# Optimization experiments

Hardware: AMD Instinct MI355X
Metric: run time of the kernel (lower is better)

Reference implementation:

```python
import jax, jax.numpy as jnp
import numpy as np

B, C, S, H, W = 1, 256, 64, 32, 128
BLOCKS, HEADS, DH = 2, 8, 32
SCALE = DH ** (-0.5)


def layer_norm(x, w, b, eps=1e-5):
    mu = jnp.mean(x, axis=-1, keepdims=True)
    var = jnp.var(x, axis=-1, keepdims=True)
    return (x - mu) * jax.lax.rsqrt(var + eps) * w + b


def generate_y_for_attn(y, u):
    # y: (B,C,H,W), u: (B,S,S) float -> (B, S^2, 2H, C)
    Bv, Cv, Hv, Wv = y.shape
    Sv = u.shape[1]
    uf = jnp.floor(u).reshape(Bv, Sv * Sv)
    u_left = jnp.clip(uf, 0, Wv - 1).astype(jnp.int32)
    u_right = jnp.clip(uf + 1, 0, Wv - 1).astype(jnp.int32)
    yf = y.reshape(Bv, Cv * Hv, Wv)

    def gather_w(idx):
        idxb = jnp.broadcast_to(idx[:, None, :], (Bv, Cv * Hv, Sv * Sv))
        return jnp.take_along_axis(yf, idxb, axis=2).reshape(Bv, Cv, Hv, Sv * Sv)

    ys = jnp.concatenate([gather_w(u_left), gather_w(u_right)], axis=2)  # (B,C,2H,S2)
    return ys.transpose(0, 3, 2, 1)  # (B, S2, 2H, C)


def cross_attention(x, y, p, i):
    # x: (B,M,C), y: (B,M,N,C)
    q = layer_norm(x, p['ln_q_w'][i], p['ln_q_b'][i]) @ p['Wq'][i]        # (B,M,HD)
    k = layer_norm(y, p['ln_k_w'][i], p['ln_k_b'][i]) @ p['Wk'][i]        # (B,M,N,HD)
    v = layer_norm(y, p['ln_v_w'][i], p['ln_v_b'][i]) @ p['Wv'][i]        # (B,M,N,HD)
    Bv, M, _ = q.shape
    N = k.shape[2]
    q = q.reshape(Bv, M, HEADS, DH)
    k = k.reshape(Bv, M, N, HEADS, DH)
    v = v.reshape(Bv, M, N, HEADS, DH)
    dot = SCALE * jnp.einsum('bmhd,bmnhd->bhmn', q, k)                    # (B,H,M,N)
    attn = jax.nn.softmax(dot, axis=-1)
    a = jnp.einsum('bhmn,bmnhd->bmhd', attn, v).reshape(Bv, M, HEADS * DH)
    z = a @ p['Wproj'][i] + p['bproj'][i]
    z = layer_norm(z, p['ln_pre_w'][i], p['ln_pre_b'][i])
    h = jax.nn.gelu(z @ p['Wm1'][i] + p['bm1'][i], approximate=False)
    z = z + (h @ p['Wm2'][i] + p['bm2'][i])
    return layer_norm(z, p['ln_post_w'][i], p['ln_post_b'][i])


def setup_inputs() -> dict:
    key = jax.random.key(0)
    ks = jax.random.split(key, 16)
    std = 0.02
    inp = {
        'grd2sat': jax.random.normal(ks[0], (B, C, S, S), jnp.float32),
        'grd_x': jax.random.normal(ks[1], (B, C, H, W), jnp.float32),
        'u': jax.random.uniform(ks[2], (B, S, S), jnp.float32) * (W - 1),
        'ln_q_w': jnp.ones((BLOCKS, C)), 'ln_q_b': jnp.zeros((BLOCKS, C)),
        'ln_k_w': jnp.ones((BLOCKS, C)), 'ln_k_b': jnp.zeros((BLOCKS, C)),
        'ln_v_w': jnp.ones((BLOCKS, C)), 'ln_v_b': jnp.zeros((BLOCKS, C)),
        'Wq': std * jax.random.normal(ks[3], (BLOCKS, C, HEADS * DH)),
        'Wk': std * jax.random.normal(ks[4], (BLOCKS, C, HEADS * DH)),
        'Wv': std * jax.random.normal(ks[5], (BLOCKS, C, HEADS * DH)),
        'Wproj': std * jax.random.normal(ks[6], (BLOCKS, HEADS * DH, C)),
        'bproj': jnp.zeros((BLOCKS, C)),
        'ln_pre_w': jnp.ones((BLOCKS, C)), 'ln_pre_b': jnp.zeros((BLOCKS, C)),
        'Wm1': std * jax.random.normal(ks[7], (BLOCKS, C, 2 * C)),
        'bm1': jnp.zeros((BLOCKS, 2 * C)),
        'Wm2': std * jax.random.normal(ks[8], (BLOCKS, 2 * C, C)),
        'bm2': jnp.zeros((BLOCKS, C)),
        'ln_post_w': jnp.ones((BLOCKS, C)), 'ln_post_b': jnp.zeros((BLOCKS, C)),
    }
    return inp


def reference(grd2sat, grd_x, u, ln_q_w, ln_q_b, ln_k_w, ln_k_b, ln_v_w, ln_v_b,
              Wq, Wk, Wv, Wproj, bproj, ln_pre_w, ln_pre_b, Wm1, bm1, Wm2, bm2,
              ln_post_w, ln_post_b):
    p = dict(ln_q_w=ln_q_w, ln_q_b=ln_q_b, ln_k_w=ln_k_w, ln_k_b=ln_k_b,
             ln_v_w=ln_v_w, ln_v_b=ln_v_b, Wq=Wq, Wk=Wk, Wv=Wv, Wproj=Wproj,
             bproj=bproj, ln_pre_w=ln_pre_w, ln_pre_b=ln_pre_b, Wm1=Wm1, bm1=bm1,
             Wm2=Wm2, bm2=bm2, ln_post_w=ln_post_w, ln_post_b=ln_post_b)
    y_attn = generate_y_for_attn(grd_x, u)               # (B, S^2, 2H, C)
    x = grd2sat.reshape(B, C, S * S).transpose(0, 2, 1)  # (B, M, C)
    for i in range(BLOCKS):
        # (Swin self-attention layer omitted; cross-attention stack only.)
        x = cross_attention(x, y_attn, p, i)
    out = x.transpose(0, 2, 1).reshape(B, C, S, S)
    # L2 normalize over channel dim
    norm = jnp.sqrt(jnp.sum(out * out, axis=1, keepdims=True))
    return out / jnp.maximum(norm, 1e-12)
```

## Files before the change

### kernel.cpp

```cpp
#include <hip/hip_runtime.h>
#include <math.h>


#define C_DIM 256
#define M_DIM 4096
#define W_DIM 128
#define H_DIM 32
#define ATT_SCALE 0.17677669529663687f

typedef __attribute__((ext_vector_type(8))) short short8;
typedef __attribute__((ext_vector_type(4))) short short4v;
typedef __attribute__((ext_vector_type(4))) float floatx4;

__device__ __forceinline__ unsigned short f2bf(float f) {
    unsigned u = __float_as_uint(f);
    unsigned r = (u + 0x7fffu + ((u >> 16) & 1u)) >> 16;
    return (unsigned short)r;
}
__device__ __forceinline__ float gelu_exact(float x) {
    return 0.5f * x * (1.0f + erff(x * 0.70710678118654752f));
}

struct PrepArgs {
    const float* grd2sat; float* xcur;
    const float* grd_x;   float* yhat;
    const float* u; int* perm; int4* chunks; int* nchunks;
    const float* win[12]; unsigned short* wout[12]; const float* wlnw[12];
    int wR[12], wC[12], wbase[13];
    const float* fW[10]; const float* flnb[10]; const float* fbase[10];
    float* fout[10];
    int fN[10], fwcol[10], focol[10];
};

__global__ __launch_bounds__(256) void prep_kernel(PrepArgs a) {
    __shared__ float smemf[9024];
    int b = blockIdx.x, t = threadIdx.x;
    if (b < 256) {
        float (*tile)[65] = (float(*)[65])smemf;
        int m0 = (b & 63) << 6, c0 = (b >> 6) << 6;
        for (int it = 0; it < 16; ++it) {
            int idx = it * 256 + t;
            int co = idx >> 6, mo = idx & 63;
            tile[co][mo] = a.grd2sat[(size_t)(c0 + co) * M_DIM + m0 + mo];
        }
        __syncthreads();
        for (int it = 0; it < 16; ++it) {
            int idx = it * 256 + t;
            int mo = idx >> 6, co = idx & 63;
            a.xcur[(size_t)(m0 + mo) * C_DIM + c0 + co] = tile[co][mo];
        }
    } else if (b < 384) {
        int idx = b - 256;
        int h = idx & 31, w0 = (idx >> 5) << 5;
        float (*tile)[33] = (float(*)[33])smemf;
        float (*ps)[32] = (float(*)[32])(smemf + 8448);
        float (*pss)[32] = (float(*)[32])(smemf + 8704);
        float* mu_s = smemf + 8960;
        float* rs_s = smemf + 8992;
        int wo = t & 31, cb = t >> 5;
        for (int it = 0; it < 32; ++it) {
            int c = it * 8 + cb;
            tile[c][wo] = a.grd_x[(size_t)c * (H_DIM * W_DIM) + h * W_DIM + w0 + wo];
        }
        __syncthreads();
        {
            int w = t & 31, part = t >> 5;
            float s = 0.f, ss = 0.f;
            for (int c = part * 32; c < part * 32 + 32; ++c) {
                float x = tile[c][w];
                s += x; ss += x * x;
            }
            ps[part][w] = s; pss[part][w] = ss;
        }
        __syncthreads();
        if (t < 32) {
            float s = 0.f, ss = 0.f;
            for (int p = 0; p < 8; ++p) { s += ps[p][t]; ss += pss[p][t]; }
            float mu = s * (1.f / 256.f);
            float var = ss * (1.f / 256.f) - mu * mu;
            mu_s[t] = mu;
            rs_s[t] = rsqrtf(var + 1e-5f);
        }
        __syncthreads();
        for (int jj = 0; jj < 32; ++jj) {
            float mu = mu_s[jj], rs = rs_s[jj];
            a.yhat[((size_t)(w0 + jj) * H_DIM + h) * C_DIM + t] =
                (tile[t][jj] - mu) * rs;
        }
    } else if (b < 1408) {
        int wI = b - 384;
        int e = 0;
        while (wI >= a.wbase[e + 1]) ++e;
        int tl = wI - a.wbase[e];
        int tilesC = a.wC[e] >> 5;
        int tr = tl / tilesC, tc = tl - tr * tilesC;
        int r0 = tr << 5, c0 = tc << 5;
        const float* in = a.win[e];
        unsigned short* out = a.wout[e];
        const float* lnw = a.wlnw[e];
        int R = a.wR[e], Cc = a.wC[e];
        float (*tile)[33] = (float(*)[33])smemf;
        int rl = t >> 3, cq = (t & 7) << 2;
        float4 v = *(const float4*)&in[(size_t)(r0 + rl) * Cc + c0 + cq];
        if (lnw) {
            float s = lnw[r0 + rl];
            v.x *= s; v.y *= s; v.z *= s; v.w *= s;
        }
        tile[rl][cq + 0] = v.x;
        tile[rl][cq + 1] = v.y;
        tile[rl][cq + 2] = v.z;
        tile[rl][cq + 3] = v.w;
        __syncthreads();
        int cl = t >> 3, rq = (t & 7) << 2;
        ushort4 o;
        o.x = f2bf(tile[rq + 0][cl]);
        o.y = f2bf(tile[rq + 1][cl]);
        o.z = f2bf(tile[rq + 2][cl]);
        o.w = f2bf(tile[rq + 3][cl]);
        *(ushort4*)&out[(size_t)(c0 + cl) * R + r0 + rq] = o;
    } else if (b < 1418) {
        int jj = b - 1408;
        int N = a.fN[jj];
        int wcol = a.fwcol[jj] + t;
        const float* W = a.fW[jj];
        const float* lb = a.flnb[jj];
        float s = a.fbase[jj] ? a.fbase[jj][wcol] : 0.f;
        for (int k = 0; k < 256; ++k) s += lb[k] * W[(size_t)k * N + wcol];
        a.fout[jj][a.focol[jj] + t] = s;
    } else {
        int* hist = (int*)smemf;
        int* cur = (int*)smemf + 128;
        unsigned short* wlb = (unsigned short*)((int*)smemf + 256);
        if (t < 128) hist[t] = 0;
        __syncthreads();
        for (int it = 0; it < 16; ++it) {
            int m = it * 256 + t;
            int wl = (int)floorf(a.u[m]);
            wl = max(0, min(wl, 126));
            wlb[m] = (unsigned short)wl;
            atomicAdd(&hist[wl], 1);
        }
        __syncthreads();
        if (t == 0) {
            int run = 0, nc = 0;
            for (int bkt = 0; bkt < 127; ++bkt) {
                int c = hist[bkt];
                cur[bkt] = run;
                int q0 = run;
                while (c > 0) {
                    int take = min(c, 32);
                    a.chunks[nc] = make_int4(bkt, q0, take, 0);
                    ++nc; q0 += take; c -= take;
                }
                run += hist[bkt];
            }
            *a.nchunks = nc;
        }
        __syncthreads();
        for (int it = 0; it < 16; ++it) {
            int m = it * 256 + t;
            int wl = wlb[m];
            int pos = atomicAdd(&cur[wl], 1);
            a.perm[pos] = m;
        }
    }
}

struct GJ {
    const float* A; const unsigned short* Bt;
    const float* bias; const float* aw; const float* ab;
    const float* rw; const float* rb; const float* res;
    float* wrz; void* out; unsigned short* out2;
    int K, N;
};

template <int LN, int EPI, int OUTM, bool WRZ>
__device__ __forceinline__ void gemm_core(const GJ& j, short (*As)[264],
                                          short (*Bs)[264], int bm, int by) {
    int t = threadIdx.x;
    int bn = by << 6;
    int wv = t >> 6, lane = t & 63;
    int mt = wv & 1, nt0 = (wv >> 1) << 1;
    int quad = lane >> 4, l16 = lane & 15;
    floatx4 acc0 = {0.f, 0.f, 0.f, 0.f};
    floatx4 acc1 = {0.f, 0.f, 0.f, 0.f};
    const int K = j.K;
    for (int kc = 0; kc < K; kc += 256) {
        if (kc) __syncthreads();
        {
            int ar = t >> 3, cq = (t & 7) << 2;
            const float* ap = j.A + (size_t)(bm + ar) * K + kc + cq;
            float4 v[8];
#pragma unroll
            for (int g = 0; g < 8; ++g) v[g] = *(const float4*)(ap + g * 32);
            if (LN >= 1) {
                float s = 0.f, ss = 0.f;
#pragma unroll
                for (int g = 0; g < 8; ++g) {
                    s += v[g].x + v[g].y + v[g].z + v[g].w;
                    ss += v[g].x * v[g].x + v[g].y * v[g].y + v[g].z * v[g].z +
                          v[g].w * v[g].w;
                }
#pragma unroll
                for (int o = 1; o < 8; o <<= 1) {
                    s += __shfl_xor(s, o, 64);
                    ss += __shfl_xor(ss, o, 64);
                }
                float mu = s * (1.f / 256.f);
                float rs = rsqrtf(ss * (1.f / 256.f) - mu * mu + 1e-5f);
#pragma unroll
                for (int g = 0; g < 8; ++g) {
                    v[g].x = (v[g].x - mu) * rs;
                    v[g].y = (v[g].y - mu) * rs;
                    v[g].z = (v[g].z - mu) * rs;
                    v[g].w = (v[g].w - mu) * rs;
                }
                if (LN == 2) {
                    float s2 = 0.f, ss2 = 0.f;
#pragma unroll
                    for (int g = 0; g < 8; ++g) {
                        float4 w4 = *(const float4*)(j.aw + cq + g * 32);
                        float4 b4 = *(const float4*)(j.ab + cq + g * 32);
                        v[g].x = v[g].x * w4.x + b4.x;
                        v[g].y = v[g].y * w4.y + b4.y;
                        v[g].z = v[g].z * w4.z + b4.z;
                        v[g].w = v[g].w * w4.w + b4.w;
                        s2 += v[g].x + v[g].y + v[g].z + v[g].w;
                        ss2 += v[g].x * v[g].x + v[g].y * v[g].y +
                               v[g].z * v[g].z + v[g].w * v[g].w;
                    }
#pragma unroll
                    for (int o = 1; o < 8; o <<= 1) {
                        s2 += __shfl_xor(s2, o, 64);
                        ss2 += __shfl_xor(ss2, o, 64);
                    }
                    float mu2 = s2 * (1.f / 256.f);
                    float rs2 = rsqrtf(ss2 * (1.f / 256.f) - mu2 * mu2 + 1e-5f);
#pragma unroll
                    for (int g = 0; g < 8; ++g) {
                        v[g].x = (v[g].x - mu2) * rs2;
                        v[g].y = (v[g].y - mu2) * rs2;
                        v[g].z = (v[g].z - mu2) * rs2;
                        v[g].w = (v[g].w - mu2) * rs2;
                    }
                }
            }
            if (WRZ) {
                if (by == 0) {
#pragma unroll
                    for (int g = 0; g < 8; ++g)
                        *(float4*)&j.wrz[(size_t)(bm + ar) * 256 + cq + g * 32] =
                            v[g];
                }
            }
#pragma unroll
            for (int g = 0; g < 8; ++g) {
                short4v o;
                o[0] = (short)f2bf(v[g].x);
                o[1] = (short)f2bf(v[g].y);
                o[2] = (short)f2bf(v[g].z);
                o[3] = (short)f2bf(v[g].w);
                *(short4v*)&As[ar][cq + g * 32] = o;
            }
        }
        {
            int br = t >> 2, cq2 = (t & 3) << 3;
            const unsigned short* bp = j.Bt + (size_t)(bn + br) * K + kc + cq2;
#pragma unroll
            for (int g = 0; g < 8; ++g)
                *(short8*)&Bs[br][cq2 + g * 32] = *(const short8*)(bp + g * 32);
        }
        __syncthreads();
#pragma unroll
        for (int k0 = 0; k0 < 8; ++k0) {
            short8 aa = *(const short8*)&As[(mt << 4) + l16][(k0 << 5) + (quad << 3)];
            short8 b0 = *(const short8*)&Bs[(nt0 << 4) + l16][(k0 << 5) + (quad << 3)];
            short8 b1 =
                *(const short8*)&Bs[((nt0 + 1) << 4) + l16][(k0 << 5) + (quad << 3)];
            acc0 = __builtin_amdgcn_mfma_f32_16x16x32_bf16(aa, b0, acc0, 0, 0, 0);
            acc1 = __builtin_amdgcn_mfma_f32_16x16x32_bf16(aa, b1, acc1, 0, 0, 0);
        }
    }
#pragma unroll
    for (int jj = 0; jj < 2; ++jj) {
        const floatx4 accv = jj ? acc1 : acc0;
        int col = bn + ((nt0 + jj) << 4) + l16;
        float bv = j.bias ? j.bias[col] : 0.f;
#pragma unroll
        for (int r = 0; r < 4; ++r) {
            int row = bm + (mt << 4) + (quad << 2) + r;
            float v = accv[r] + bv;
            if (EPI == 1) v = gelu_exact(v);
            if (EPI == 2)
                v += j.res[(size_t)row * 256 + col] * j.rw[col] + j.rb[col];
            if (OUTM == 0) {
                ((float*)j.out)[(size_t)row * j.N + col] = v;
            } else if (OUTM == 1) {
                ((unsigned short*)j.out)[(size_t)row * 256 + col] = f2bf(v);
            } else {
                if (col < 256)
                    ((unsigned short*)j.out)[(size_t)row * 256 + col] = f2bf(v);
                else
                    j.out2[(size_t)(col - 256) * M_DIM + row] = f2bf(v);
            }
        }
    }
}

template <int MODE>
__global__ __launch_bounds__(256) void gemm_mode(GJ j0, GJ j1) {
    __shared__ short As[32][264];
    __shared__ short Bs[64][264];
    int bm = blockIdx.x << 5;
    if (MODE == 0) {
        if ((int)blockIdx.y < 4) gemm_core<1, 0, 1, false>(j0, As, Bs, bm, blockIdx.y);
        else gemm_core<0, 0, 2, false>(j1, As, Bs, bm, blockIdx.y - 4);
    } else if (MODE == 1) {
        if ((int)blockIdx.y < 4) gemm_core<2, 0, 1, false>(j0, As, Bs, bm, blockIdx.y);
        else gemm_core<0, 0, 2, false>(j1, As, Bs, bm, blockIdx.y - 4);
    } else if (MODE == 2) {
        gemm_core<0, 0, 0, false>(j0, As, Bs, bm, blockIdx.y);
    } else if (MODE == 3) {
        gemm_core<1, 1, 0, true>(j0, As, Bs, bm, blockIdx.y);
    } else {
        gemm_core<0, 2, 0, false>(j0, As, Bs, bm, blockIdx.y);
    }
}

__global__ __launch_bounds__(256) void attn_kernel(
    const unsigned short* __restrict__ Qb, const unsigned short* __restrict__ Kt,
    const unsigned short* __restrict__ Vt, const int* __restrict__ perm,
    const int4* __restrict__ chunks, const int* __restrict__ nchunks,
    float* __restrict__ Ao) {
    __shared__ short Qs[32][264];
    __shared__ short Ks[64][264];
    __shared__ short VsT[256][72];
    __shared__ float S[32][69];
    __shared__ short Pb[32][72];
    __shared__ int gperm[32];
    if ((int)blockIdx.x >= *nchunks) return;
    int4 cd = chunks[blockIdx.x];
    int wl = cd.x, qstart = cd.y, qcnt = cd.z;
    int t = threadIdx.x;
    if (t < 32) gperm[t] = (t < qcnt) ? perm[qstart + t] : 0;
    {
        int q = t >> 3, p = t & 7;
        if (q < qcnt) {
            const uint4* src =
                (const uint4*)(Qb + (size_t)perm[qstart + q] * 256 + (p << 5));
#pragma unroll
            for (int c = 0; c < 4; ++c) *(uint4*)&Qs[q][(p << 5) + (c << 3)] = src[c];
        } else {
            uint4 z = make_uint4(0, 0, 0, 0);
#pragma unroll
            for (int c = 0; c < 4; ++c) *(uint4*)&Qs[q][(p << 5) + (c << 3)] = z;
        }
    }
    {
        int n = t >> 2, p = t & 3;
        const uint4* src = (const uint4*)(Kt + ((size_t)(wl * 32 + n)) * 256 + (p << 6));
#pragma unroll
        for (int c = 0; c < 8; ++c) *(uint4*)&Ks[n][(p << 6) + (c << 3)] = src[c];
    }
    {
        const uint4* src = (const uint4*)(Vt + (size_t)t * M_DIM + (wl << 5));
#pragma unroll
        for (int c = 0; c < 8; ++c) *(uint4*)&VsT[t][c << 3] = src[c];
    }
    __syncthreads();
    int wv = t >> 6, lane = t & 63, quad = lane >> 4, l16 = lane & 15;
    int mtS = wv & 1, ntS0 = (wv >> 1) << 1;
    int mtP = wv & 1, ntP = wv >> 1;
    int sq = t >> 3, sg = t & 7;
#pragma unroll 1
    for (int h = 0; h < 8; ++h) {
        {
            short8 aa = *(const short8*)&Qs[(mtS << 4) + l16][(h << 5) + (quad << 3)];
            short8 b0 = *(const short8*)&Ks[(ntS0 << 4) + l16][(h << 5) + (quad << 3)];
            short8 b1 =
                *(const short8*)&Ks[((ntS0 + 1) << 4) + l16][(h << 5) + (quad << 3)];
            floatx4 z = {0.f, 0.f, 0.f, 0.f};
            floatx4 c0 = __builtin_amdgcn_mfma_f32_16x16x32_bf16(aa, b0, z, 0, 0, 0);
            floatx4 c1 = __builtin_amdgcn_mfma_f32_16x16x32_bf16(aa, b1, z, 0, 0, 0);
#pragma unroll
            for (int r = 0; r < 4; ++r) {
                int row = (mtS << 4) + (quad << 2) + r;
                S[row][(ntS0 << 4) + l16] = c0[r];
                S[row][((ntS0 + 1) << 4) + l16] = c1[r];
            }
        }
        __syncthreads();
        {
            float e[8];
            float s = 0.f;
#pragma unroll
            for (int c = 0; c < 8; ++c) {
                e[c] = __expf(S[sq][(sg << 3) + c] * ATT_SCALE);
                s += e[c];
            }
            s += __shfl_xor(s, 1, 64);
            s += __shfl_xor(s, 2, 64);
            s += __shfl_xor(s, 4, 64);
            float ri = 1.f / s;
#pragma unroll
            for (int c = 0; c < 8; ++c)
                Pb[sq][(sg << 3) + c] = (short)f2bf(e[c] * ri);
        }
        __syncthreads();
        {
            floatx4 acc = {0.f, 0.f, 0.f, 0.f};
#pragma unroll
            for (int ks = 0; ks < 2; ++ks) {
                short8 aa =
                    *(const short8*)&Pb[(mtP << 4) + l16][(ks << 5) + (quad << 3)];
                short8 bb = *(const short8*)&VsT[(h << 5) + (ntP << 4) + l16]
                                                [(ks << 5) + (quad << 3)];
                acc = __builtin_amdgcn_mfma_f32_16x16x32_bf16(aa, bb, acc, 0, 0, 0);
            }
#pragma unroll
            for (int r = 0; r < 4; ++r) {
                int q = (mtP << 4) + (quad << 2) + r;
                if (q < qcnt)
                    Ao[(size_t)gperm[q] * C_DIM + (h << 5) + (ntP << 4) + l16] =
                        acc[r];
            }
        }
        __syncthreads();
    }
}

__global__ __launch_bounds__(256) void out_kernel(const float* __restrict__ X,
                                                  const float* __restrict__ w,
                                                  const float* __restrict__ b,
                                                  float* __restrict__ out) {
    __shared__ float tile[64][65];
    int t = threadIdx.x;
    int mo = t >> 2, q = t & 3;
    int m0 = blockIdx.x << 6;
    const float* p = X + (size_t)(m0 + mo) * C_DIM + (q << 6);
    float4 v[16];
    float s = 0.f, ss = 0.f;
#pragma unroll
    for (int c = 0; c < 16; ++c) {
        v[c] = *(const float4*)(p + c * 4);
        s += v[c].x + v[c].y + v[c].z + v[c].w;
        ss += v[c].x * v[c].x + v[c].y * v[c].y + v[c].z * v[c].z + v[c].w * v[c].w;
    }
    s += __shfl_xor(s, 1, 64); s += __shfl_xor(s, 2, 64);
    ss += __shfl_xor(ss, 1, 64); ss += __shfl_xor(ss, 2, 64);
    float mu = s * (1.f / 256.f);
    float rs = rsqrtf(ss * (1.f / 256.f) - mu * mu + 1e-5f);
    float ss2 = 0.f;
#pragma unroll
    for (int c = 0; c < 16; ++c) {
        float4 w4 = *(const float4*)&w[(q << 6) + c * 4];
        float4 b4 = *(const float4*)&b[(q << 6) + c * 4];
        v[c].x = (v[c].x - mu) * rs * w4.x + b4.x;
        v[c].y = (v[c].y - mu) * rs * w4.y + b4.y;
        v[c].z = (v[c].z - mu) * rs * w4.z + b4.z;
        v[c].w = (v[c].w - mu) * rs * w4.w + b4.w;
        ss2 += v[c].x * v[c].x + v[c].y * v[c].y + v[c].z * v[c].z + v[c].w * v[c].w;
    }
    ss2 += __shfl_xor(ss2, 1, 64); ss2 += __shfl_xor(ss2, 2, 64);
    float sc = 1.f / fmaxf(sqrtf(ss2), 1e-12f);
    for (int cc = 0; cc < 4; ++cc) {
        if (q == cc) {
#pragma unroll
            for (int c = 0; c < 16; ++c) {
                tile[mo][c * 4 + 0] = v[c].x * sc;
                tile[mo][c * 4 + 1] = v[c].y * sc;
                tile[mo][c * 4 + 2] = v[c].z * sc;
                tile[mo][c * 4 + 3] = v[c].w * sc;
            }
        }
        __syncthreads();
        for (int it = 0; it < 16; ++it) {
            int idx = it * 256 + t;
            int co = idx >> 6, mr = idx & 63;
            out[(size_t)((cc << 6) + co) * M_DIM + m0 + mr] = tile[mr][co];
        }
        __syncthreads();
    }
}

extern "C" void kernel_launch(void* const* d_in, const int* in_sizes, int n_in,
                              void* d_out, int out_size, void* d_ws, size_t ws_size,
                              hipStream_t stream) {
    const float* grd2sat = (const float*)d_in[0];
    const float* grd_x   = (const float*)d_in[1];
    const float* u       = (const float*)d_in[2];
    const float* ln_q_w  = (const float*)d_in[3];
    const float* ln_q_b  = (const float*)d_in[4];
    const float* ln_k_w  = (const float*)d_in[5];
    const float* ln_k_b  = (const float*)d_in[6];
    const float* ln_v_w  = (const float*)d_in[7];
    const float* ln_v_b  = (const float*)d_in[8];
    const float* Wq      = (const float*)d_in[9];
    const float* Wk      = (const float*)d_in[10];
    const float* Wv      = (const float*)d_in[11];
    const float* Wproj   = (const float*)d_in[12];
    const float* bproj   = (const float*)d_in[13];
    const float* ln_pre_w = (const float*)d_in[14];
    const float* ln_pre_b = (const float*)d_in[15];
    const float* Wm1     = (const float*)d_in[16];
    const float* bm1     = (const float*)d_in[17];
    const float* Wm2     = (const float*)d_in[18];
    const float* bm2     = (const float*)d_in[19];
    const float* ln_post_w = (const float*)d_in[20];
    const float* ln_post_b = (const float*)d_in[21];

    float* ws   = (float*)d_ws;
    float* yhat = ws;
    float* xcur = ws + 1048576;
    float* zq   = ws + 2097152;
    float* abuf = ws + 3145728;
    float* hbuf = ws + 4194304;
    float* zbuf = ws + 6291456;
    unsigned short* Qb   = (unsigned short*)(ws + 7340032);
    unsigned short* Ktab = (unsigned short*)(ws + 7864320);
    unsigned short* Vt   = (unsigned short*)(ws + 8388608);
    unsigned short* Bt   = (unsigned short*)(ws + 8912896);
    float* biasbuf = ws + 9961472;
    int*  perm    = (int*)(ws + 9965568);
    int4* chunks  = (int4*)(ws + 9969664);
    int*  nchunks = (int*)(ws + 9970688);
    const size_t BS = 524288;
    const size_t OQ = 0, OKV = 65536, OP = 196608, OM1 = 262144, OM2 = 393216;

    dim3 b256(256);

    PrepArgs pa;
    pa.grd2sat = grd2sat; pa.xcur = xcur;
    pa.grd_x = grd_x;     pa.yhat = yhat;
    pa.u = u; pa.perm = perm; pa.chunks = chunks; pa.nchunks = nchunks;
    {
        int base = 0;
        for (int i = 0; i < 2; ++i) {
            int e = 6 * i;
            unsigned short* bt = Bt + i * BS;
            pa.win[e+0] = Wq + i * 65536;    pa.wout[e+0] = bt + OQ;
            pa.wlnw[e+0] = ln_q_w + i * 256; pa.wR[e+0] = 256; pa.wC[e+0] = 256;
            pa.win[e+1] = Wk + i * 65536;    pa.wout[e+1] = bt + OKV;
            pa.wlnw[e+1] = ln_k_w + i * 256; pa.wR[e+1] = 256; pa.wC[e+1] = 256;
            pa.win[e+2] = Wv + i * 65536;    pa.wout[e+2] = bt + OKV + 65536;
            pa.wlnw[e+2] = ln_v_w + i * 256; pa.wR[e+2] = 256; pa.wC[e+2] = 256;
            pa.win[e+3] = Wproj + i * 65536; pa.wout[e+3] = bt + OP;
            pa.wlnw[e+3] = nullptr;          pa.wR[e+3] = 256; pa.wC[e+3] = 256;
            pa.win[e+4] = Wm1 + i * 131072;  pa.wout[e+4] = bt + OM1;
            pa.wlnw[e+4] = ln_pre_w + i * 256; pa.wR[e+4] = 256; pa.wC[e+4] = 512;
            pa.win[e+5] = Wm2 + i * 131072;  pa.wout[e+5] = bt + OM2;
            pa.wlnw[e+5] = nullptr;          pa.wR[e+5] = 512; pa.wC[e+5] = 256;
        }
        for (int e = 0; e < 12; ++e) {
            pa.wbase[e] = base;
            base += (pa.wR[e] >> 5) * (pa.wC[e] >> 5);
        }
        pa.wbase[12] = base;
        for (int i = 0; i < 2; ++i) {
            int jb = 5 * i;
            float* bb = biasbuf + i * 1280;
            pa.fW[jb+0] = Wq + i * 65536; pa.flnb[jb+0] = ln_q_b + i * 256;
            pa.fbase[jb+0] = nullptr; pa.fout[jb+0] = bb;
            pa.fN[jb+0] = 256; pa.fwcol[jb+0] = 0; pa.focol[jb+0] = 0;
            pa.fW[jb+1] = Wk + i * 65536; pa.flnb[jb+1] = ln_k_b + i * 256;
            pa.fbase[jb+1] = nullptr; pa.fout[jb+1] = bb + 256;
            pa.fN[jb+1] = 256; pa.fwcol[jb+1] = 0; pa.focol[jb+1] = 0;
            pa.fW[jb+2] = Wv + i * 65536; pa.flnb[jb+2] = ln_v_b + i * 256;
            pa.fbase[jb+2] = nullptr; pa.fout[jb+2] = bb + 256;
            pa.fN[jb+2] = 256; pa.fwcol[jb+2] = 0; pa.focol[jb+2] = 256;
            pa.fW[jb+3] = Wm1 + i * 131072; pa.flnb[jb+3] = ln_pre_b + i * 256;
            pa.fbase[jb+3] = bm1 + i * 512; pa.fout[jb+3] = bb + 768;
            pa.fN[jb+3] = 512; pa.fwcol[jb+3] = 0; pa.focol[jb+3] = 0;
            pa.fW[jb+4] = Wm1 + i * 131072; pa.flnb[jb+4] = ln_pre_b + i * 256;
            pa.fbase[jb+4] = bm1 + i * 512; pa.fout[jb+4] = bb + 768;
            pa.fN[jb+4] = 512; pa.fwcol[jb+4] = 256; pa.focol[jb+4] = 256;
        }
    }
    prep_kernel<<<1419, b256, 0, stream>>>(pa);

    for (int i = 0; i < 2; ++i) {
        const unsigned short* bt = Bt + i * BS;
        float* bb = biasbuf + i * 1280;
        GJ jq = {};
        jq.A = xcur; jq.Bt = bt + OQ; jq.bias = bb;
        if (i == 1) { jq.aw = ln_post_w; jq.ab = ln_post_b; }
        jq.out = Qb; jq.K = 256; jq.N = 256;
        GJ jkv = {};
        jkv.A = yhat; jkv.Bt = bt + OKV; jkv.bias = bb + 256;
        jkv.out = Ktab; jkv.out2 = Vt; jkv.K = 256; jkv.N = 512;
        if (i == 0) gemm_mode<0><<<dim3(128, 12), b256, 0, stream>>>(jq, jkv);
        else        gemm_mode<1><<<dim3(128, 12), b256, 0, stream>>>(jq, jkv);

        attn_kernel<<<255, b256, 0, stream>>>(Qb, Ktab, Vt, perm, chunks,
                                              nchunks, abuf);

        GJ jp = {};
        jp.A = abuf; jp.Bt = bt + OP; jp.bias = bproj + i * 256;
        jp.out = zq; jp.K = 256; jp.N = 256;
        gemm_mode<2><<<dim3(128, 4), b256, 0, stream>>>(jp, jp);

        GJ jm1 = {};
        jm1.A = zq; jm1.Bt = bt + OM1; jm1.bias = bb + 768;
        jm1.out = hbuf; jm1.wrz = zbuf; jm1.K = 256; jm1.N = 512;
        gemm_mode<3><<<dim3(128, 8), b256, 0, stream>>>(jm1, jm1);

        GJ jm2 = {};
        jm2.A = hbuf; jm2.Bt = bt + OM2; jm2.bias = bm2 + i * 256;
        jm2.res = zbuf; jm2.rw = ln_pre_w + i * 256; jm2.rb = ln_pre_b + i * 256;
        jm2.out = xcur; jm2.K = 512; jm2.N = 256;
        gemm_mode<4><<<dim3(128, 4), b256, 0, stream>>>(jm2, jm2);
    }
    out_kernel<<<64, b256, 0, stream>>>(xcur, ln_post_w + 256, ln_post_b + 256,
                                        (float*)d_out);
}
```

Baseline: 220.8 us.

## Hoist block-1 K/V GEMM into block 0, bf16 intermediates, split attention heads

Both blocks' K/V projections read the same input yhat, so they are now computed in one launch during block 0 into separate buffers, and block 1 launches only the Q projection. The attention kernel drops its LDS staging of Q/K/V, reads them directly from global memory, splits the 8 heads across a second grid dimension for more blocks, and writes its output in bf16. The MLP hidden activation and the attention output are stored as bf16 and read by the following GEMMs through a new bf16 A-operand path, cutting global traffic. The cost is extra rounding to bf16 and uncached, possibly uncoalesced global loads inside attention.

```diff
diff --git a/kernel.cpp b/kernel.cpp
--- a/kernel.cpp
+++ b/kernel.cpp
@@ -167,14 +167,14 @@
 }
 
 struct GJ {
-    const float* A; const unsigned short* Bt;
+    const void* A; const unsigned short* Bt;
     const float* bias; const float* aw; const float* ab;
     const float* rw; const float* rb; const float* res;
     float* wrz; void* out; unsigned short* out2;
     int K, N;
 };
 
-template <int LN, int EPI, int OUTM, bool WRZ>
+template <int LN, int EPI, int OUTM, bool WRZ, bool ABF16>
 __device__ __forceinline__ void gemm_core(const GJ& j, short (*As)[264],
                                           short (*Bs)[264], int bm, int by) {
     int t = threadIdx.x;
@@ -187,9 +187,16 @@
     const int K = j.K;
     for (int kc = 0; kc < K; kc += 256) {
         if (kc) __syncthreads();
-        {
+        if (ABF16) {
+            int ar = t >> 3, cq = (t & 7) << 5;
+            const unsigned short* ap =
+                (const unsigned short*)j.A + (size_t)(bm + ar) * K + kc + cq;
+#pragma unroll
+            for (int c = 0; c < 4; ++c)
+                *(uint4*)&As[ar][cq + (c << 3)] = *(const uint4*)(ap + (c << 3));
+        } else {
             int ar = t >> 3, cq = (t & 7) << 2;
-            const float* ap = j.A + (size_t)(bm + ar) * K + kc + cq;
+            const float* ap = (const float*)j.A + (size_t)(bm + ar) * K + kc + cq;
             float4 v[8];
 #pragma unroll
             for (int g = 0; g < 8; ++g) v[g] = *(const float4*)(ap + g * 32);
@@ -296,7 +303,7 @@
             if (OUTM == 0) {
                 ((float*)j.out)[(size_t)row * j.N + col] = v;
             } else if (OUTM == 1) {
-                ((unsigned short*)j.out)[(size_t)row * 256 + col] = f2bf(v);
+                ((unsigned short*)j.out)[(size_t)row * j.N + col] = f2bf(v);
             } else {
                 if (col < 256)
                     ((unsigned short*)j.out)[(size_t)row * 256 + col] = f2bf(v);
@@ -308,22 +315,25 @@
 }
 
 template <int MODE>
-__global__ __launch_bounds__(256) void gemm_mode(GJ j0, GJ j1) {
+__global__ __launch_bounds__(256) void gemm_mode(GJ j0, GJ j1, GJ j2) {
     __shared__ short As[32][264];
     __shared__ short Bs[64][264];
     int bm = blockIdx.x << 5;
     if (MODE == 0) {
-        if ((int)blockIdx.y < 4) gemm_core<1, 0, 1, false>(j0, As, Bs, bm, blockIdx.y);
-        else gemm_core<0, 0, 2, false>(j1, As, Bs, bm, blockIdx.y - 4);
+        if ((int)blockIdx.y < 4)
+            gemm_core<1, 0, 1, false, false>(j0, As, Bs, bm, blockIdx.y);
+        else if ((int)blockIdx.y < 12)
+            gemm_core<0, 0, 2, false, false>(j1, As, Bs, bm, blockIdx.y - 4);
+        else
+            gemm_core<0, 0, 2, false, false>(j2, As, Bs, bm, blockIdx.y - 12);
     } else if (MODE == 1) {
-        if ((int)blockIdx.y < 4) gemm_core<2, 0, 1, false>(j0, As, Bs, bm, blockIdx.y);
-        else gemm_core<0, 0, 2, false>(j1, As, Bs, bm, blockIdx.y - 4);
+        gemm_core<2, 0, 1, false, false>(j0, As, Bs, bm, blockIdx.y);
     } else if (MODE == 2) {
-        gemm_core<0, 0, 0, false>(j0, As, Bs, bm, blockIdx.y);
+        gemm_core<0, 0, 0, false, true>(j0, As, Bs, bm, blockIdx.y);
     } else if (MODE == 3) {
-        gemm_core<1, 1, 0, true>(j0, As, Bs, bm, blockIdx.y);
+        gemm_core<1, 1, 1, true, false>(j0, As, Bs, bm, blockIdx.y);
     } else {
-        gemm_core<0, 2, 0, false>(j0, As, Bs, bm, blockIdx.y);
+        gemm_core<0, 2, 0, false, true>(j0, As, Bs, bm, blockIdx.y);
     }
 }
 
@@ -331,10 +341,7 @@
     const unsigned short* __restrict__ Qb, const unsigned short* __restrict__ Kt,
     const unsigned short* __restrict__ Vt, const int* __restrict__ perm,
     const int4* __restrict__ chunks, const int* __restrict__ nchunks,
-    float* __restrict__ Ao) {
-    __shared__ short Qs[32][264];
-    __shared__ short Ks[64][264];
-    __shared__ short VsT[256][72];
+    unsigned short* __restrict__ Ao) {
     __shared__ float S[32][69];
     __shared__ short Pb[32][72];
     __shared__ int gperm[32];
@@ -342,51 +349,31 @@
     int4 cd = chunks[blockIdx.x];
     int wl = cd.x, qstart = cd.y, qcnt = cd.z;
     int t = threadIdx.x;
-    if (t < 32) gperm[t] = (t < qcnt) ? perm[qstart + t] : 0;
-    {
-        int q = t >> 3, p = t & 7;
-        if (q < qcnt) {
-            const uint4* src =
-                (const uint4*)(Qb + (size_t)perm[qstart + q] * 256 + (p << 5));
-#pragma unroll
-            for (int c = 0; c < 4; ++c) *(uint4*)&Qs[q][(p << 5) + (c << 3)] = src[c];
-        } else {
-            uint4 z = make_uint4(0, 0, 0, 0);
-#pragma unroll
-            for (int c = 0; c < 4; ++c) *(uint4*)&Qs[q][(p << 5) + (c << 3)] = z;
-        }
-    }
-    {
-        int n = t >> 2, p = t & 3;
-        const uint4* src = (const uint4*)(Kt + ((size_t)(wl * 32 + n)) * 256 + (p << 6));
-#pragma unroll
-        for (int c = 0; c < 8; ++c) *(uint4*)&Ks[n][(p << 6) + (c << 3)] = src[c];
-    }
-    {
-        const uint4* src = (const uint4*)(Vt + (size_t)t * M_DIM + (wl << 5));
-#pragma unroll
-        for (int c = 0; c < 8; ++c) *(uint4*)&VsT[t][c << 3] = src[c];
-    }
+    if (t < 32) gperm[t] = (t < qcnt) ? perm[qstart + t] : perm[qstart];
     __syncthreads();
     int wv = t >> 6, lane = t & 63, quad = lane >> 4, l16 = lane & 15;
-    int mtS = wv & 1, ntS0 = (wv >> 1) << 1;
-    int mtP = wv & 1, ntP = wv >> 1;
+    int mt = wv & 1, nt0 = (wv >> 1) << 1;
+    int ntP = wv >> 1;
+    const unsigned short* qp = Qb + (size_t)gperm[(mt << 4) + l16] * 256;
+    const unsigned short* kp0 =
+        Kt + ((size_t)((wl << 5) + (nt0 << 4) + l16)) * 256;
+    const unsigned short* kp1 = kp0 + (16 * 256);
     int sq = t >> 3, sg = t & 7;
+    int hb = (int)blockIdx.y << 2;
 #pragma unroll 1
-    for (int h = 0; h < 8; ++h) {
+    for (int h = hb; h < hb + 4; ++h) {
         {
-            short8 aa = *(const short8*)&Qs[(mtS << 4) + l16][(h << 5) + (quad << 3)];
-            short8 b0 = *(const short8*)&Ks[(ntS0 << 4) + l16][(h << 5) + (quad << 3)];
-            short8 b1 =
-                *(const short8*)&Ks[((ntS0 + 1) << 4) + l16][(h << 5) + (quad << 3)];
+            short8 aa = *(const short8*)(qp + (h << 5) + (quad << 3));
+            short8 b0 = *(const short8*)(kp0 + (h << 5) + (quad << 3));
+            short8 b1 = *(const short8*)(kp1 + (h << 5) + (quad << 3));
             floatx4 z = {0.f, 0.f, 0.f, 0.f};
             floatx4 c0 = __builtin_amdgcn_mfma_f32_16x16x32_bf16(aa, b0, z, 0, 0, 0);
             floatx4 c1 = __builtin_amdgcn_mfma_f32_16x16x32_bf16(aa, b1, z, 0, 0, 0);
 #pragma unroll
             for (int r = 0; r < 4; ++r) {
-                int row = (mtS << 4) + (quad << 2) + r;
-                S[row][(ntS0 << 4) + l16] = c0[r];
-                S[row][((ntS0 + 1) << 4) + l16] = c1[r];
+                int row = (mt << 4) + (quad << 2) + r;
+                S[row][(nt0 << 4) + l16] = c0[r];
+                S[row][((nt0 + 1) << 4) + l16] = c1[r];
             }
         }
         __syncthreads();
@@ -408,24 +395,24 @@
         }
         __syncthreads();
         {
+            const unsigned short* vp =
+                Vt + ((size_t)((h << 5) + (ntP << 4) + l16)) * M_DIM + (wl << 5);
             floatx4 acc = {0.f, 0.f, 0.f, 0.f};
 #pragma unroll
             for (int ks = 0; ks < 2; ++ks) {
-                short8 aa =
-                    *(const short8*)&Pb[(mtP << 4) + l16][(ks << 5) + (quad << 3)];
-                short8 bb = *(const short8*)&VsT[(h << 5) + (ntP << 4) + l16]
-                                                [(ks << 5) + (quad << 3)];
-                acc = __builtin_amdgcn_mfma_f32_16x16x32_bf16(aa, bb, acc, 0, 0, 0);
+                short8 pa =
+                    *(const short8*)&Pb[(mt << 4) + l16][(ks << 5) + (quad << 3)];
+                short8 vb = *(const short8*)(vp + (ks << 5) + (quad << 3));
+                acc = __builtin_amdgcn_mfma_f32_16x16x32_bf16(pa, vb, acc, 0, 0, 0);
             }
 #pragma unroll
             for (int r = 0; r < 4; ++r) {
-                int q = (mtP << 4) + (quad << 2) + r;
+                int q = (mt << 4) + (quad << 2) + r;
                 if (q < qcnt)
-                    Ao[(size_t)gperm[q] * C_DIM + (h << 5) + (ntP << 4) + l16] =
-                        acc[r];
-            }
-        }
-        __syncthreads();
+                    Ao[(size_t)gperm[q] * 256 + (h << 5) + (ntP << 4) + l16] =
+                        f2bf(acc[r]);
+            }
+        }
     }
 }
 
@@ -513,17 +500,19 @@
     float* yhat = ws;
     float* xcur = ws + 1048576;
     float* zq   = ws + 2097152;
-    float* abuf = ws + 3145728;
-    float* hbuf = ws + 4194304;
-    float* zbuf = ws + 6291456;
-    unsigned short* Qb   = (unsigned short*)(ws + 7340032);
-    unsigned short* Ktab = (unsigned short*)(ws + 7864320);
-    unsigned short* Vt   = (unsigned short*)(ws + 8388608);
-    unsigned short* Bt   = (unsigned short*)(ws + 8912896);
-    float* biasbuf = ws + 9961472;
-    int*  perm    = (int*)(ws + 9965568);
-    int4* chunks  = (int4*)(ws + 9969664);
-    int*  nchunks = (int*)(ws + 9970688);
+    float* zbuf = ws + 3145728;
+    unsigned short* hbuf = (unsigned short*)(ws + 4194304);
+    unsigned short* Qb   = (unsigned short*)(ws + 5242880);
+    unsigned short* abuf = (unsigned short*)(ws + 5767168);
+    unsigned short* Ktab0 = (unsigned short*)(ws + 6291456);
+    unsigned short* Vt0   = (unsigned short*)(ws + 6815744);
+    unsigned short* Ktab1 = (unsigned short*)(ws + 7340032);
+    unsigned short* Vt1   = (unsigned short*)(ws + 7864320);
+    unsigned short* Bt    = (unsigned short*)(ws + 8388608);
+    float* biasbuf = ws + 8912896;
+    int*  perm    = (int*)(ws + 8915456);
+    int4* chunks  = (int4*)(ws + 8919552);
+    int*  nchunks = (int*)(ws + 8921600);
     const size_t BS = 524288;
     const size_t OQ = 0, OKV = 65536, OP = 196608, OM1 = 262144, OM2 = 393216;
 
@@ -578,37 +567,47 @@
     }
     prep_kernel<<<1419, b256, 0, stream>>>(pa);
 
+    GJ jz = {};
     for (int i = 0; i < 2; ++i) {
         const unsigned short* bt = Bt + i * BS;
         float* bb = biasbuf + i * 1280;
+        unsigned short* Kt = i ? Ktab1 : Ktab0;
+        unsigned short* Vt = i ? Vt1 : Vt0;
+
         GJ jq = {};
         jq.A = xcur; jq.Bt = bt + OQ; jq.bias = bb;
         if (i == 1) { jq.aw = ln_post_w; jq.ab = ln_post_b; }
         jq.out = Qb; jq.K = 256; jq.N = 256;
-        GJ jkv = {};
-        jkv.A = yhat; jkv.Bt = bt + OKV; jkv.bias = bb + 256;
-        jkv.out = Ktab; jkv.out2 = Vt; jkv.K = 256; jkv.N = 512;
-        if (i == 0) gemm_mode<0><<<dim3(128, 12), b256, 0, stream>>>(jq, jkv);
-        else        gemm_mode<1><<<dim3(128, 12), b256, 0, stream>>>(jq, jkv);
-
-        attn_kernel<<<255, b256, 0, stream>>>(Qb, Ktab, Vt, perm, chunks,
-                                              nchunks, abuf);
+        if (i == 0) {
+            GJ jkv0 = {};
+            jkv0.A = yhat; jkv0.Bt = Bt + OKV; jkv0.bias = biasbuf + 256;
+            jkv0.out = Ktab0; jkv0.out2 = Vt0; jkv0.K = 256; jkv0.N = 512;
+            GJ jkv1 = {};
+            jkv1.A = yhat; jkv1.Bt = Bt + BS + OKV; jkv1.bias = biasbuf + 1280 + 256;
+            jkv1.out = Ktab1; jkv1.out2 = Vt1; jkv1.K = 256; jkv1.N = 512;
+            gemm_mode<0><<<dim3(128, 20), b256, 0, stream>>>(jq, jkv0, jkv1);
+        } else {
+            gemm_mode<1><<<dim3(128, 4), b256, 0, stream>>>(jq, jz, jz);
+        }
+
+        attn_kernel<<<dim3(384, 2), b256, 0, stream>>>(Qb, Kt, Vt, perm, chunks,
+                                                       nchunks, abuf);
 
         GJ jp = {};
         jp.A = abuf; jp.Bt = bt + OP; jp.bias = bproj + i * 256;
         jp.out = zq; jp.K = 256; jp.N = 256;
-        gemm_mode<2><<<dim3(128, 4), b256, 0, stream>>>(jp, jp);
+        gemm_mode<2><<<dim3(128, 4), b256, 0, stream>>>(jp, jz, jz);
 
         GJ jm1 = {};
         jm1.A = zq; jm1.Bt = bt + OM1; jm1.bias = bb + 768;
         jm1.out = hbuf; jm1.wrz = zbuf; jm1.K = 256; jm1.N = 512;
-        gemm_mode<3><<<dim3(128, 8), b256, 0, stream>>>(jm1, jm1);
+        gemm_mode<3><<<dim3(128, 8), b256, 0, stream>>>(jm1, jz, jz);
 
         GJ jm2 = {};
         jm2.A = hbuf; jm2.Bt = bt + OM2; jm2.bias = bm2 + i * 256;
         jm2.res = zbuf; jm2.rw = ln_pre_w + i * 256; jm2.rb = ln_pre_b + i * 256;
         jm2.out = xcur; jm2.K = 512; jm2.N = 256;
-        gemm_mode<4><<<dim3(128, 4), b256, 0, stream>>>(jm2, jm2);
+        gemm_mode<4><<<dim3(128, 4), b256, 0, stream>>>(jm2, jz, jz);
     }
     out_kernel<<<64, b256, 0, stream>>>(xcur, ln_post_w + 256, ln_post_b + 256,
                                         (float*)d_out);
```

Result: faster. 216.4 us (-2.0%).
